# Performance work log

Measured on AMD Instinct MI355X. Metric: run time of the kernel, lower is better.

## Reference

```python
import jax, jax.numpy as jnp
import numpy as np
from jax import lax

B, S, D = 8, 1024, 128

def setup_inputs() -> dict:
    key = jax.random.key(0)
    ks = jax.random.split(key, 6)
    scale = 1.0 / np.sqrt(D)
    return {
        "x": jax.random.normal(ks[0], (B, S, D), dtype=jnp.float32),
        "Wk": jax.random.normal(ks[1], (D, D), dtype=jnp.float32) * scale,
        "Wv": jax.random.normal(ks[2], (D, D), dtype=jnp.float32) * scale,
        "Wq": jax.random.normal(ks[3], (D, D), dtype=jnp.float32) * scale,
        "Wg": jax.random.normal(ks[4], (D, 3), dtype=jnp.float32) * scale,
        "bg": jnp.zeros((3,), dtype=jnp.float32),
    }

def reference(x, Wk, Wv, Wq, Wg, bg):
    b, s, d = x.shape
    k = x @ Wk  # [b,s,d]
    v = x @ Wv
    q = x @ Wq
    gates = jax.nn.sigmoid(x @ Wg + bg)  # [b,s,3]
    alpha, eta, theta = gates[..., 0], gates[..., 1], gates[..., 2]  # [b,s]

    M0 = jnp.zeros((b, d, d), dtype=x.dtype)
    S0 = jnp.zeros((b, d, d), dtype=x.dtype)

    # time-major scan inputs
    xs = (jnp.swapaxes(k, 0, 1), jnp.swapaxes(v, 0, 1), jnp.swapaxes(q, 0, 1),
          jnp.swapaxes(alpha, 0, 1), jnp.swapaxes(eta, 0, 1), jnp.swapaxes(theta, 0, 1))

    def scan_fn(carry, inp):
        M_prev, S_prev = carry
        kt, vt, qt, at, et, tt = inp  # kt/vt/qt: [b,d]; at/et/tt: [b]
        # NOTE: original einsum 'bd,bdd->bd' takes the DIAGONAL of M (faithful)
        diagM = jnp.einsum('bdd->bd', M_prev)  # [b,d]
        yt = qt * diagM
        pred = kt * diagM
        error = pred - vt
        grad = kt[:, :, None] * error[:, None, :]  # outer product [b,d,d]
        S_new = et[:, None, None] * S_prev - tt[:, None, None] * grad
        M_new = (1.0 - at[:, None, None]) * M_prev + S_new
        return (M_new, S_new), yt

    (M_final, S_final), outputs = lax.scan(scan_fn, (M0, S0), xs)
    outputs = jnp.swapaxes(outputs, 0, 1)  # [b,s,d]
    return (outputs, (M_final, S_final))
```

## Files before the change

### kernel.cpp

```cpp
#include <hip/hip_runtime.h>
#include <math.h>

#define NB 8
#define NS 1024
#define ND 128
#define NC 64
#define NL 16

#define OFF_K  0u
#define OFF_Q  1048576u
#define OFF_V  2097152u
#define OFF_E  3145728u
#define OFF_GA 4194304u
#define OFF_GE 4202496u
#define OFF_GT 4210688u
#define OFF_W  4218880u
#define OFF_C  4227072u
#define OFF_P  4235264u

#define PL_A00 (OFF_P)
#define PL_A01 (OFF_P +  65536u)
#define PL_A10 (OFF_P + 131072u)
#define PL_A11 (OFF_P + 196608u)
#define PL_B0  (OFF_P + 262144u)
#define PL_B1  (OFF_P + 327680u)
#define PL_MST (OFF_P + 393216u)
#define PL_SST (OFF_P + 458752u)
#define PL_WCA (OFF_P + 524288u)
#define PL_WCB (OFF_P + 524800u)
#define PL_WCD (OFF_P + 525312u)
#define PL_WRQ (OFF_P + 525824u)
#define PL_WRP (OFF_P + 526336u)
#define PL_WRA (OFF_P + 526848u)
#define OFF_WT (OFF_P + 532480u)
#define WT_LO  49152u

typedef short bf16x8 __attribute__((ext_vector_type(8)));
typedef float f32x4  __attribute__((ext_vector_type(4)));

static __device__ __forceinline__ unsigned short f2bf(float f) {
    unsigned u = __builtin_bit_cast(unsigned, f);
    unsigned r = (u + 0x7FFFu + ((u >> 16) & 1u)) >> 16;
    return (unsigned short)r;
}
static __device__ __forceinline__ float bf2f(unsigned short h) {
    unsigned u = ((unsigned)h) << 16;
    return __builtin_bit_cast(float, u);
}
static __device__ __forceinline__ void split2(float a, float b,
                                              unsigned& hi, unsigned& lo) {
    unsigned short ah = f2bf(a), bh = f2bf(b);
    float ar = a - bf2f(ah), br = b - bf2f(bh);
    hi = (unsigned)ah | ((unsigned)bh << 16);
    lo = (unsigned)f2bf(ar) | ((unsigned)f2bf(br) << 16);
}

__global__ __launch_bounds__(256) void wtprep_kernel(
    const float* __restrict__ Wk, const float* __restrict__ Wv,
    const float* __restrict__ Wq, unsigned short* __restrict__ wtg)
{
    const int m    = blockIdx.x >> 4;
    const int cgrp = blockIdx.x & 15;
    const int tid  = threadIdx.x;
    const int cl   = tid >> 5;
    const int h    = tid & 31;
    const int c    = cgrp * 8 + cl;
    const float* W = (m == 0) ? Wk : (m == 1) ? Wv : Wq;

    float f[4];
#pragma unroll
    for (int i = 0; i < 4; ++i)
        f[i] = W[(h * 4 + i) * ND + c];
    uint2 hi, lo;
    split2(f[0], f[1], hi.x, lo.x);
    split2(f[2], f[3], hi.y, lo.y);
    const unsigned base = (unsigned)m * 16384u + (unsigned)c * 128u + (unsigned)h * 4u;
    *(uint2*)&wtg[base]         = hi;
    *(uint2*)&wtg[WT_LO + base] = lo;
}

__global__ __launch_bounds__(256) void proj_mfma(
    const float* __restrict__ x, const unsigned short* __restrict__ wtg,
    const float* __restrict__ Wg, const float* __restrict__ bg,
    float* __restrict__ Kb, float* __restrict__ Vb, float* __restrict__ Qb,
    float* __restrict__ ga, float* __restrict__ ge, float* __restrict__ gt)
{
    __shared__ unsigned short xs_hi[32 * 136];
    __shared__ unsigned short xs_lo[32 * 136];
    __shared__ unsigned short wt_hi[64 * 136];
    __shared__ unsigned short wt_lo[64 * 136];

    const int tid  = threadIdx.x;
    const int bid  = blockIdx.x;
    const int m    = bid >> 9;
    const int rt   = (bid >> 1) & 255;
    const int ch   = bid & 1;
    const int row0 = rt * 32;

    const float4* x4 = (const float4*)x;
#pragma unroll
    for (int l = 0; l < 4; ++l) {
        int idx = tid + l * 256;
        int r = idx >> 5, kq = idx & 31;
        float4 f = x4[(row0 + r) * 32 + kq];
        uint2 hi, lo;
        split2(f.x, f.y, hi.x, lo.x);
        split2(f.z, f.w, hi.y, lo.y);
        *(uint2*)&xs_hi[r * 136 + kq * 4] = hi;
        *(uint2*)&xs_lo[r * 136 + kq * 4] = lo;
    }
    const uint4* wh4 = (const uint4*)(wtg + m * 16384 + ch * 64 * 128);
    const uint4* wl4 = (const uint4*)(wtg + WT_LO + m * 16384 + ch * 64 * 128);
#pragma unroll
    for (int l = 0; l < 4; ++l) {
        int idx = tid + l * 256;
        int c = idx >> 4, u = idx & 15;
        *(uint4*)&wt_hi[c * 136 + u * 8] = wh4[c * 16 + u];
        *(uint4*)&wt_lo[c * 136 + u * 8] = wl4[c * 16 + u];
    }
    __syncthreads();

    const int wid  = tid >> 6;
    const int lane = tid & 63;
    const int rg   = wid >> 1;
    const int cg   = wid & 1;
    const int lrow = rg * 16 + (lane & 15);
    const int quad = lane >> 4;

    f32x4 acc[2];
    acc[0] = (f32x4){0.f, 0.f, 0.f, 0.f};
    acc[1] = (f32x4){0.f, 0.f, 0.f, 0.f};

#pragma unroll
    for (int kk = 0; kk < 4; ++kk) {
        bf16x8 ah = *(const bf16x8*)&xs_hi[lrow * 136 + kk * 32 + quad * 8];
        bf16x8 al = *(const bf16x8*)&xs_lo[lrow * 136 + kk * 32 + quad * 8];
#pragma unroll
        for (int ct = 0; ct < 2; ++ct) {
            int cl = cg * 32 + ct * 16 + (lane & 15);
            bf16x8 bh = *(const bf16x8*)&wt_hi[cl * 136 + kk * 32 + quad * 8];
            bf16x8 bl = *(const bf16x8*)&wt_lo[cl * 136 + kk * 32 + quad * 8];
            acc[ct] = __builtin_amdgcn_mfma_f32_16x16x32_bf16(ah, bh, acc[ct], 0, 0, 0);
            acc[ct] = __builtin_amdgcn_mfma_f32_16x16x32_bf16(ah, bl, acc[ct], 0, 0, 0);
            acc[ct] = __builtin_amdgcn_mfma_f32_16x16x32_bf16(al, bh, acc[ct], 0, 0, 0);
        }
    }

    float* dst = (m == 0) ? Kb : (m == 1) ? Vb : Qb;
#pragma unroll
    for (int ct = 0; ct < 2; ++ct) {
        int ocol = ch * 64 + cg * 32 + ct * 16 + (lane & 15);
#pragma unroll
        for (int r4 = 0; r4 < 4; ++r4) {
            int orow = row0 + rg * 16 + quad * 4 + r4;
            dst[orow * ND + ocol] = acc[ct][r4];
        }
    }

    if (m == 0 && ch == 0 && tid < 96) {
        int r = tid / 3, j = tid % 3;
        float z = bg[j];
        const float* xr = x + (row0 + r) * ND;
#pragma unroll 4
        for (int i = 0; i < ND; ++i)
            z = fmaf(xr[i], Wg[i * 3 + j], z);
        float gate = 1.0f / (1.0f + expf(-z));
        int row = row0 + r;
        float* gd = (j == 0) ? ga : (j == 1) ? ge : gt;
        gd[row] = gate;
    }
}

__global__ __launch_bounds__(128) void scan_phase1(
    const float* __restrict__ Kb, const float* __restrict__ Vb,
    const float* __restrict__ ga, const float* __restrict__ ge,
    const float* __restrict__ gt, float* __restrict__ ws)
{
    __shared__ float la[NL], le[NL], lt[NL];
    const int tid = threadIdx.x;
    const int b   = blockIdx.x >> 6;
    const int c   = blockIdx.x & 63;
    const int t0  = c * NL;
    const int g0  = b * NS + t0;

    if (tid < 16)       la[tid]      = ga[g0 + tid];
    else if (tid < 32)  le[tid - 16] = ge[g0 + tid - 16];
    else if (tid < 48)  lt[tid - 32] = gt[g0 + tid - 32];
    __syncthreads();

    const int d = tid;
    float A00 = 1.f, A01 = 0.f, A10 = 0.f, A11 = 1.f, B0 = 0.f, B1 = 0.f;
    int base = g0 * ND + d;
#pragma unroll
    for (int t = 0; t < NL; ++t) {
        float k = Kb[base], v = Vb[base];
        float a = la[t], e = le[t], th = lt[t];
        float tk = th * k;
        float gg = -tk * k;
        float h  = tk * v;
        float p  = (1.0f - a) + gg;
        float u0 = e * A10;
        float u1 = e * A11;
        float u2 = fmaf(e, B1, h);
        float n00 = fmaf(p, A00, u0), n10 = fmaf(gg, A00, u0);
        float n01 = fmaf(p, A01, u1), n11 = fmaf(gg, A01, u1);
        float nb0 = fmaf(p, B0, u2),  nb1 = fmaf(gg, B0, u2);
        A00 = n00; A01 = n01; A10 = n10; A11 = n11; B0 = nb0; B1 = nb1;
        base += ND;
    }
    const int pidx = (b * NC + c) * ND + d;
    ws[PL_A00 + pidx] = A00;
    ws[PL_A01 + pidx] = A01;
    ws[PL_A10 + pidx] = A10;
    ws[PL_A11 + pidx] = A11;
    ws[PL_B0  + pidx] = B0;
    ws[PL_B1  + pidx] = B1;

    if (tid == 0) {
        float al = 1.f, be = 1.f, de = 0.f;
#pragma unroll
        for (int t = NL - 1; t >= 0; --t) {
            float e1 = le[t];
            float o1 = 1.0f - la[t];
            de = fmaf(e1, de, o1 * be);
            al *= e1;
            be *= o1;
        }
        ws[PL_WCA + b * NC + c] = al;
        ws[PL_WCB + b * NC + c] = be;
        ws[PL_WCD + b * NC + c] = de;
    }
}

__global__ __launch_bounds__(64) void scan_phase2(float* __restrict__ ws)
{
    const int tid = threadIdx.x;
    if (blockIdx.x < 16) {
        const int b = blockIdx.x >> 1;
        const int d = (blockIdx.x & 1) * 64 + tid;
        float m = 0.f, s = 0.f;
        int idx = (b * NC) * ND + d;
#pragma unroll 4
        for (int c = 0; c < NC; ++c) {
            ws[PL_MST + idx] = m;
            ws[PL_SST + idx] = s;
            float A00 = ws[PL_A00 + idx], A01 = ws[PL_A01 + idx];
            float A10 = ws[PL_A10 + idx], A11 = ws[PL_A11 + idx];
            float B0  = ws[PL_B0  + idx], B1  = ws[PL_B1  + idx];
            float nm = fmaf(A00, m, fmaf(A01, s, B0));
            float ns = fmaf(A10, m, fmaf(A11, s, B1));
            m = nm; s = ns;
            idx += ND;
        }
    } else if (tid < 8) {
        const int b = tid;
        float Qp = 1.f, P = 1.f, A = 1.f;
        for (int c = NC - 1; c >= 0; --c) {
            ws[PL_WRQ + b * NC + c] = Qp;
            ws[PL_WRP + b * NC + c] = P;
            ws[PL_WRA + b * NC + c] = A;
            float al = ws[PL_WCA + b * NC + c];
            float be = ws[PL_WCB + b * NC + c];
            float de = ws[PL_WCD + b * NC + c];
            float nA = fmaf(al, A, de * P);
            Qp *= al; P *= be; A = nA;
        }
    }
}

__global__ __launch_bounds__(128) void scan_phase3(
    const float* __restrict__ Kb, const float* __restrict__ Vb,
    const float* __restrict__ Qb,
    const float* __restrict__ ga, const float* __restrict__ ge,
    const float* __restrict__ gt,
    float* __restrict__ out, float* __restrict__ errb,
    float* __restrict__ wb,  float* __restrict__ cb,
    float* __restrict__ ws)
{
    __shared__ float la[NL], le[NL], lt[NL];
    const int tid = threadIdx.x;
    const int b   = blockIdx.x >> 6;
    const int c   = blockIdx.x & 63;
    const int t0  = c * NL;
    const int g0  = b * NS + t0;

    if (tid < 16)       la[tid]      = ga[g0 + tid];
    else if (tid < 32)  le[tid - 16] = ge[g0 + tid - 16];
    else if (tid < 48)  lt[tid - 32] = gt[g0 + tid - 32];
    __syncthreads();

    const int d = tid;
    const int pidx = (b * NC + c) * ND + d;
    float m = ws[PL_MST + pidx];
    float s = ws[PL_SST + pidx];
    int base = g0 * ND + d;
#pragma unroll
    for (int t = 0; t < NL; ++t) {
        float k = Kb[base], v = Vb[base], q = Qb[base];
        float a = la[t], e = le[t], th = lt[t];
        float err = fmaf(k, m, -v);
        out[base]  = q * m;
        errb[base] = err;
        float tk = th * k;
        float u  = fmaf(-(tk * k), m, tk * v);
        s = fmaf(e, s, u);
        m = fmaf(1.0f - a, m, s);
        base += ND;
    }

    if (tid == 0) {
        float Qp = ws[PL_WRQ + b * NC + c];
        float P  = ws[PL_WRP + b * NC + c];
        float A  = ws[PL_WRA + b * NC + c];
#pragma unroll
        for (int t = NL - 1; t >= 0; --t) {
            wb[g0 + t] = -lt[t] * Qp;
            cb[g0 + t] = -lt[t] * A;
            float e1 = le[t];
            float o1 = 1.0f - la[t];
            Qp *= e1;
            P  *= o1;
            A   = fmaf(e1, A, P);
        }
    }
}

__global__ __launch_bounds__(256) void finalgemm_kernel(
    const float* __restrict__ Kb, const float* __restrict__ errb,
    const float* __restrict__ wb, const float* __restrict__ cb,
    float* __restrict__ outMS)
{
    __shared__ float ks[64 * 16];
    __shared__ float wcs[64 * 2];
    const int tid = threadIdx.x;
    const int bid = blockIdx.x;
    const int b   = bid >> 7;
    const int tc  = (bid >> 3) & 15;
    const int rg  = bid & 7;
    const int bt0 = b * NS + tc * 64;

    {
        int tl = tid >> 2, r4 = tid & 3;
        *(float4*)&ks[tl * 16 + r4 * 4] =
            *(const float4*)&Kb[(bt0 + tl) * ND + rg * 16 + r4 * 4];
    }
    if (tid < 64) {
        wcs[tid * 2]     = wb[bt0 + tid];
        wcs[tid * 2 + 1] = cb[bt0 + tid];
    }
    __syncthreads();

    const int j = tid & 127;
    const int h = tid >> 7;
    float accM[8], accS[8];
#pragma unroll
    for (int i = 0; i < 8; ++i) { accM[i] = 0.f; accS[i] = 0.f; }

    int ebase = bt0 * ND + j;
#pragma unroll 4
    for (int t = 0; t < 64; ++t) {
        float ej = errb[ebase];
        float2 wc = *(const float2*)&wcs[t * 2];
        float wej = wc.x * ej, cej = wc.y * ej;
        float4 k0 = *(const float4*)&ks[t * 16 + h * 8];
        float4 k1 = *(const float4*)&ks[t * 16 + h * 8 + 4];
        accS[0] = fmaf(k0.x, wej, accS[0]); accM[0] = fmaf(k0.x, cej, accM[0]);
        accS[1] = fmaf(k0.y, wej, accS[1]); accM[1] = fmaf(k0.y, cej, accM[1]);
        accS[2] = fmaf(k0.z, wej, accS[2]); accM[2] = fmaf(k0.z, cej, accM[2]);
        accS[3] = fmaf(k0.w, wej, accS[3]); accM[3] = fmaf(k0.w, cej, accM[3]);
        accS[4] = fmaf(k1.x, wej, accS[4]); accM[4] = fmaf(k1.x, cej, accM[4]);
        accS[5] = fmaf(k1.y, wej, accS[5]); accM[5] = fmaf(k1.y, cej, accM[5]);
        accS[6] = fmaf(k1.z, wej, accS[6]); accM[6] = fmaf(k1.z, cej, accM[6]);
        accS[7] = fmaf(k1.w, wej, accS[7]); accM[7] = fmaf(k1.w, cej, accM[7]);
        ebase += ND;
    }

    const int robase = rg * 16 + h * 8;
#pragma unroll
    for (int i = 0; i < 8; ++i) {
        int off = b * (ND * ND) + (robase + i) * ND + j;
        atomicAdd(&outMS[off], accM[i]);
        atomicAdd(&outMS[131072u + off], accS[i]);
    }
}

extern "C" void kernel_launch(void* const* d_in, const int* in_sizes, int n_in,
                              void* d_out, int out_size, void* d_ws, size_t ws_size,
                              hipStream_t stream) {
    const float* x  = (const float*)d_in[0];
    const float* Wk = (const float*)d_in[1];
    const float* Wv = (const float*)d_in[2];
    const float* Wq = (const float*)d_in[3];
    const float* Wg = (const float*)d_in[4];
    const float* bg = (const float*)d_in[5];
    float* out = (float*)d_out;
    float* ws  = (float*)d_ws;

    float* Kb  = ws + OFF_K;
    float* Qb  = ws + OFF_Q;
    float* Vb  = ws + OFF_V;
    float* Eb  = ws + OFF_E;
    float* ga  = ws + OFF_GA;
    float* ge  = ws + OFF_GE;
    float* gt  = ws + OFF_GT;
    float* wbf = ws + OFF_W;
    float* cbf = ws + OFF_C;
    unsigned short* wtg = (unsigned short*)(ws + OFF_WT);

    hipMemsetAsync(out + 1048576u, 0, 262144u * sizeof(float), stream);

    wtprep_kernel<<<48, 256, 0, stream>>>(Wk, Wv, Wq, wtg);
    proj_mfma<<<1536, 256, 0, stream>>>(x, wtg, Wg, bg,
                                        Kb, Vb, Qb, ga, ge, gt);
    scan_phase1<<<NB * NC, 128, 0, stream>>>(Kb, Vb, ga, ge, gt, ws);
    scan_phase2<<<17, 64, 0, stream>>>(ws);
    scan_phase3<<<NB * NC, 128, 0, stream>>>(Kb, Vb, Qb, ga, ge, gt,
                                             out, Eb, wbf, cbf, ws);
    finalgemm_kernel<<<1024, 256, 0, stream>>>(Kb, Eb, wbf, cbf,
                                               out + 1048576u);
}
```

Baseline: 119.0 us.

## Fuse scan phases and final GEMM into one cooperative kernel with grid syncs

Replaces the separate scan_phase1/2/3 and finalgemm launches with a single cooperative kernel of 512 blocks that uses grid.sync between phases. K/V/Q values are kept in registers from phase 1 to phase 3, and the output memset is folded into wtprep. The final reduction is retiled so each block covers 32 rows instead of 16. This removes launch overhead and repeated K/V loads, but adds grid-wide barrier costs, raises register pressure, and leaves half of each block's threads idle during the scan phases.

```diff
diff --git a/kernel.cpp b/kernel.cpp
--- a/kernel.cpp
+++ b/kernel.cpp
@@ -1,5 +1,8 @@
 #include <hip/hip_runtime.h>
+#include <hip/hip_cooperative_groups.h>
 #include <math.h>
+
+namespace cg = cooperative_groups;
 
 #define NB 8
 #define NS 1024
@@ -57,7 +60,8 @@
 
 __global__ __launch_bounds__(256) void wtprep_kernel(
     const float* __restrict__ Wk, const float* __restrict__ Wv,
-    const float* __restrict__ Wq, unsigned short* __restrict__ wtg)
+    const float* __restrict__ Wq, unsigned short* __restrict__ wtg,
+    float* __restrict__ outMS)
 {
     const int m    = blockIdx.x >> 4;
     const int cgrp = blockIdx.x & 15;
@@ -77,6 +81,14 @@
     const unsigned base = (unsigned)m * 16384u + (unsigned)c * 128u + (unsigned)h * 4u;
     *(uint2*)&wtg[base]         = hi;
     *(uint2*)&wtg[WT_LO + base] = lo;
+
+    const int gidx = blockIdx.x * 256 + tid;
+    const float4 z = {0.f, 0.f, 0.f, 0.f};
+#pragma unroll
+    for (int l = 0; l < 6; ++l) {
+        int i4 = gidx + l * 12288;
+        if (i4 < 65536) ((float4*)outMS)[i4] = z;
+    }
 }
 
 __global__ __launch_bounds__(256) void proj_mfma(
@@ -171,15 +183,25 @@
     }
 }
 
-__global__ __launch_bounds__(128) void scan_phase1(
+__global__ __launch_bounds__(256, 2) void fused_scan(
     const float* __restrict__ Kb, const float* __restrict__ Vb,
+    const float* __restrict__ Qb,
     const float* __restrict__ ga, const float* __restrict__ ge,
-    const float* __restrict__ gt, float* __restrict__ ws)
+    const float* __restrict__ gt,
+    float* __restrict__ out, float* __restrict__ errb,
+    float* __restrict__ wb,  float* __restrict__ cb,
+    float* __restrict__ ws,  float* __restrict__ outMS)
 {
     __shared__ float la[NL], le[NL], lt[NL];
+    __shared__ float ks[64 * 32];
+    __shared__ float wcs[64 * 2];
+
+    cg::grid_group grid = cg::this_grid();
+
     const int tid = threadIdx.x;
-    const int b   = blockIdx.x >> 6;
-    const int c   = blockIdx.x & 63;
+    const int bid = blockIdx.x;
+    const int b   = bid >> 6;
+    const int c   = bid & 63;
     const int t0  = c * NL;
     const int g0  = b * NS + t0;
 
@@ -188,34 +210,36 @@
     else if (tid < 48)  lt[tid - 32] = gt[g0 + tid - 32];
     __syncthreads();
 
-    const int d = tid;
-    float A00 = 1.f, A01 = 0.f, A10 = 0.f, A11 = 1.f, B0 = 0.f, B1 = 0.f;
-    int base = g0 * ND + d;
-#pragma unroll
-    for (int t = 0; t < NL; ++t) {
-        float k = Kb[base], v = Vb[base];
-        float a = la[t], e = le[t], th = lt[t];
-        float tk = th * k;
-        float gg = -tk * k;
-        float h  = tk * v;
-        float p  = (1.0f - a) + gg;
-        float u0 = e * A10;
-        float u1 = e * A11;
-        float u2 = fmaf(e, B1, h);
-        float n00 = fmaf(p, A00, u0), n10 = fmaf(gg, A00, u0);
-        float n01 = fmaf(p, A01, u1), n11 = fmaf(gg, A01, u1);
-        float nb0 = fmaf(p, B0, u2),  nb1 = fmaf(gg, B0, u2);
-        A00 = n00; A01 = n01; A10 = n10; A11 = n11; B0 = nb0; B1 = nb1;
-        base += ND;
-    }
-    const int pidx = (b * NC + c) * ND + d;
-    ws[PL_A00 + pidx] = A00;
-    ws[PL_A01 + pidx] = A01;
-    ws[PL_A10 + pidx] = A10;
-    ws[PL_A11 + pidx] = A11;
-    ws[PL_B0  + pidx] = B0;
-    ws[PL_B1  + pidx] = B1;
-
+    float k[NL], v[NL], q[NL];
+    if (tid < 128) {
+        const int d = tid;
+        float A00 = 1.f, A01 = 0.f, A10 = 0.f, A11 = 1.f, B0 = 0.f, B1 = 0.f;
+        int base = g0 * ND + d;
+#pragma unroll
+        for (int t = 0; t < NL; ++t) {
+            k[t] = Kb[base]; v[t] = Vb[base]; q[t] = Qb[base];
+            float a = la[t], e = le[t], th = lt[t];
+            float tk = th * k[t];
+            float gg = -tk * k[t];
+            float h  = tk * v[t];
+            float p  = (1.0f - a) + gg;
+            float u0 = e * A10;
+            float u1 = e * A11;
+            float u2 = fmaf(e, B1, h);
+            float n00 = fmaf(p, A00, u0), n10 = fmaf(gg, A00, u0);
+            float n01 = fmaf(p, A01, u1), n11 = fmaf(gg, A01, u1);
+            float nb0 = fmaf(p, B0, u2),  nb1 = fmaf(gg, B0, u2);
+            A00 = n00; A01 = n01; A10 = n10; A11 = n11; B0 = nb0; B1 = nb1;
+            base += ND;
+        }
+        const int pidx = (b * NC + c) * ND + d;
+        ws[PL_A00 + pidx] = A00;
+        ws[PL_A01 + pidx] = A01;
+        ws[PL_A10 + pidx] = A10;
+        ws[PL_A11 + pidx] = A11;
+        ws[PL_B0  + pidx] = B0;
+        ws[PL_B1  + pidx] = B1;
+    }
     if (tid == 0) {
         float al = 1.f, be = 1.f, de = 0.f;
 #pragma unroll
@@ -230,84 +254,64 @@
         ws[PL_WCB + b * NC + c] = be;
         ws[PL_WCD + b * NC + c] = de;
     }
-}
-
-__global__ __launch_bounds__(64) void scan_phase2(float* __restrict__ ws)
-{
-    const int tid = threadIdx.x;
-    if (blockIdx.x < 16) {
-        const int b = blockIdx.x >> 1;
-        const int d = (blockIdx.x & 1) * 64 + tid;
-        float m = 0.f, s = 0.f;
-        int idx = (b * NC) * ND + d;
+
+    grid.sync();
+
+    if (bid < 16) {
+        if (tid < 64) {
+            const int b2 = bid >> 1;
+            const int d  = (bid & 1) * 64 + tid;
+            float m = 0.f, s = 0.f;
+            int idx = (b2 * NC) * ND + d;
 #pragma unroll 4
-        for (int c = 0; c < NC; ++c) {
-            ws[PL_MST + idx] = m;
-            ws[PL_SST + idx] = s;
-            float A00 = ws[PL_A00 + idx], A01 = ws[PL_A01 + idx];
-            float A10 = ws[PL_A10 + idx], A11 = ws[PL_A11 + idx];
-            float B0  = ws[PL_B0  + idx], B1  = ws[PL_B1  + idx];
-            float nm = fmaf(A00, m, fmaf(A01, s, B0));
-            float ns = fmaf(A10, m, fmaf(A11, s, B1));
-            m = nm; s = ns;
-            idx += ND;
-        }
-    } else if (tid < 8) {
-        const int b = tid;
+            for (int cc = 0; cc < NC; ++cc) {
+                ws[PL_MST + idx] = m;
+                ws[PL_SST + idx] = s;
+                float A00 = ws[PL_A00 + idx], A01 = ws[PL_A01 + idx];
+                float A10 = ws[PL_A10 + idx], A11 = ws[PL_A11 + idx];
+                float B0  = ws[PL_B0  + idx], B1  = ws[PL_B1  + idx];
+                float nm = fmaf(A00, m, fmaf(A01, s, B0));
+                float ns = fmaf(A10, m, fmaf(A11, s, B1));
+                m = nm; s = ns;
+                idx += ND;
+            }
+        }
+    } else if (bid == 16 && tid < 8) {
+        const int b2 = tid;
         float Qp = 1.f, P = 1.f, A = 1.f;
-        for (int c = NC - 1; c >= 0; --c) {
-            ws[PL_WRQ + b * NC + c] = Qp;
-            ws[PL_WRP + b * NC + c] = P;
-            ws[PL_WRA + b * NC + c] = A;
-            float al = ws[PL_WCA + b * NC + c];
-            float be = ws[PL_WCB + b * NC + c];
-            float de = ws[PL_WCD + b * NC + c];
+        for (int cc = NC - 1; cc >= 0; --cc) {
+            ws[PL_WRQ + b2 * NC + cc] = Qp;
+            ws[PL_WRP + b2 * NC + cc] = P;
+            ws[PL_WRA + b2 * NC + cc] = A;
+            float al = ws[PL_WCA + b2 * NC + cc];
+            float be = ws[PL_WCB + b2 * NC + cc];
+            float de = ws[PL_WCD + b2 * NC + cc];
             float nA = fmaf(al, A, de * P);
             Qp *= al; P *= be; A = nA;
         }
     }
-}
-
-__global__ __launch_bounds__(128) void scan_phase3(
-    const float* __restrict__ Kb, const float* __restrict__ Vb,
-    const float* __restrict__ Qb,
-    const float* __restrict__ ga, const float* __restrict__ ge,
-    const float* __restrict__ gt,
-    float* __restrict__ out, float* __restrict__ errb,
-    float* __restrict__ wb,  float* __restrict__ cb,
-    float* __restrict__ ws)
-{
-    __shared__ float la[NL], le[NL], lt[NL];
-    const int tid = threadIdx.x;
-    const int b   = blockIdx.x >> 6;
-    const int c   = blockIdx.x & 63;
-    const int t0  = c * NL;
-    const int g0  = b * NS + t0;
-
-    if (tid < 16)       la[tid]      = ga[g0 + tid];
-    else if (tid < 32)  le[tid - 16] = ge[g0 + tid - 16];
-    else if (tid < 48)  lt[tid - 32] = gt[g0 + tid - 32];
-    __syncthreads();
-
-    const int d = tid;
-    const int pidx = (b * NC + c) * ND + d;
-    float m = ws[PL_MST + pidx];
-    float s = ws[PL_SST + pidx];
-    int base = g0 * ND + d;
-#pragma unroll
-    for (int t = 0; t < NL; ++t) {
-        float k = Kb[base], v = Vb[base], q = Qb[base];
-        float a = la[t], e = le[t], th = lt[t];
-        float err = fmaf(k, m, -v);
-        out[base]  = q * m;
-        errb[base] = err;
-        float tk = th * k;
-        float u  = fmaf(-(tk * k), m, tk * v);
-        s = fmaf(e, s, u);
-        m = fmaf(1.0f - a, m, s);
-        base += ND;
-    }
-
+
+    grid.sync();
+
+    if (tid < 128) {
+        const int d = tid;
+        const int pidx = (b * NC + c) * ND + d;
+        float m = ws[PL_MST + pidx];
+        float s = ws[PL_SST + pidx];
+        int base = g0 * ND + d;
+#pragma unroll
+        for (int t = 0; t < NL; ++t) {
+            float a = la[t], e = le[t], th = lt[t];
+            float err = fmaf(k[t], m, -v[t]);
+            out[base]  = q[t] * m;
+            errb[base] = err;
+            float tk = th * k[t];
+            float u  = fmaf(-(tk * k[t]), m, tk * v[t]);
+            s = fmaf(e, s, u);
+            m = fmaf(1.0f - a, m, s);
+            base += ND;
+        }
+    }
     if (tid == 0) {
         float Qp = ws[PL_WRQ + b * NC + c];
         float P  = ws[PL_WRP + b * NC + c];
@@ -323,26 +327,20 @@
             A   = fmaf(e1, A, P);
         }
     }
-}
-
-__global__ __launch_bounds__(256) void finalgemm_kernel(
-    const float* __restrict__ Kb, const float* __restrict__ errb,
-    const float* __restrict__ wb, const float* __restrict__ cb,
-    float* __restrict__ outMS)
-{
-    __shared__ float ks[64 * 16];
-    __shared__ float wcs[64 * 2];
-    const int tid = threadIdx.x;
-    const int bid = blockIdx.x;
-    const int b   = bid >> 7;
-    const int tc  = (bid >> 3) & 15;
-    const int rg  = bid & 7;
-    const int bt0 = b * NS + tc * 64;
-
-    {
-        int tl = tid >> 2, r4 = tid & 3;
-        *(float4*)&ks[tl * 16 + r4 * 4] =
-            *(const float4*)&Kb[(bt0 + tl) * ND + rg * 16 + r4 * 4];
+
+    grid.sync();
+
+    const int b2  = bid >> 6;
+    const int tc  = (bid >> 2) & 15;
+    const int rh  = bid & 3;
+    const int bt0 = b2 * NS + tc * 64;
+
+#pragma unroll
+    for (int l = 0; l < 2; ++l) {
+        int idx = tid + l * 256;
+        int tl = idx >> 3, r4 = idx & 7;
+        *(float4*)&ks[tl * 32 + r4 * 4] =
+            *(const float4*)&Kb[(bt0 + tl) * ND + rh * 32 + r4 * 4];
     }
     if (tid < 64) {
         wcs[tid * 2]     = wb[bt0 + tid];
@@ -352,33 +350,31 @@
 
     const int j = tid & 127;
     const int h = tid >> 7;
-    float accM[8], accS[8];
-#pragma unroll
-    for (int i = 0; i < 8; ++i) { accM[i] = 0.f; accS[i] = 0.f; }
+    float accM[16], accS[16];
+#pragma unroll
+    for (int i = 0; i < 16; ++i) { accM[i] = 0.f; accS[i] = 0.f; }
 
     int ebase = bt0 * ND + j;
-#pragma unroll 4
+#pragma unroll 2
     for (int t = 0; t < 64; ++t) {
         float ej = errb[ebase];
-        float2 wc = *(const float2*)&wcs[t * 2];
-        float wej = wc.x * ej, cej = wc.y * ej;
-        float4 k0 = *(const float4*)&ks[t * 16 + h * 8];
-        float4 k1 = *(const float4*)&ks[t * 16 + h * 8 + 4];
-        accS[0] = fmaf(k0.x, wej, accS[0]); accM[0] = fmaf(k0.x, cej, accM[0]);
-        accS[1] = fmaf(k0.y, wej, accS[1]); accM[1] = fmaf(k0.y, cej, accM[1]);
-        accS[2] = fmaf(k0.z, wej, accS[2]); accM[2] = fmaf(k0.z, cej, accM[2]);
-        accS[3] = fmaf(k0.w, wej, accS[3]); accM[3] = fmaf(k0.w, cej, accM[3]);
-        accS[4] = fmaf(k1.x, wej, accS[4]); accM[4] = fmaf(k1.x, cej, accM[4]);
-        accS[5] = fmaf(k1.y, wej, accS[5]); accM[5] = fmaf(k1.y, cej, accM[5]);
-        accS[6] = fmaf(k1.z, wej, accS[6]); accM[6] = fmaf(k1.z, cej, accM[6]);
-        accS[7] = fmaf(k1.w, wej, accS[7]); accM[7] = fmaf(k1.w, cej, accM[7]);
+        float2 wc2 = *(const float2*)&wcs[t * 2];
+        float wej = wc2.x * ej, cej = wc2.y * ej;
+#pragma unroll
+        for (int w = 0; w < 4; ++w) {
+            float4 kw = *(const float4*)&ks[t * 32 + h * 16 + w * 4];
+            accS[w*4+0] = fmaf(kw.x, wej, accS[w*4+0]); accM[w*4+0] = fmaf(kw.x, cej, accM[w*4+0]);
+            accS[w*4+1] = fmaf(kw.y, wej, accS[w*4+1]); accM[w*4+1] = fmaf(kw.y, cej, accM[w*4+1]);
+            accS[w*4+2] = fmaf(kw.z, wej, accS[w*4+2]); accM[w*4+2] = fmaf(kw.z, cej, accM[w*4+2]);
+            accS[w*4+3] = fmaf(kw.w, wej, accS[w*4+3]); accM[w*4+3] = fmaf(kw.w, cej, accM[w*4+3]);
+        }
         ebase += ND;
     }
 
-    const int robase = rg * 16 + h * 8;
-#pragma unroll
-    for (int i = 0; i < 8; ++i) {
-        int off = b * (ND * ND) + (robase + i) * ND + j;
+    const int rb = rh * 32 + h * 16;
+#pragma unroll
+    for (int i = 0; i < 16; ++i) {
+        int off = b2 * (ND * ND) + (rb + i) * ND + j;
         atomicAdd(&outMS[off], accM[i]);
         atomicAdd(&outMS[131072u + off], accS[i]);
     }
@@ -405,17 +401,17 @@
     float* gt  = ws + OFF_GT;
     float* wbf = ws + OFF_W;
     float* cbf = ws + OFF_C;
+    float* outMS = out + 1048576u;
     unsigned short* wtg = (unsigned short*)(ws + OFF_WT);
 
-    hipMemsetAsync(out + 1048576u, 0, 262144u * sizeof(float), stream);
-
-    wtprep_kernel<<<48, 256, 0, stream>>>(Wk, Wv, Wq, wtg);
+    wtprep_kernel<<<48, 256, 0, stream>>>(Wk, Wv, Wq, wtg, outMS);
     proj_mfma<<<1536, 256, 0, stream>>>(x, wtg, Wg, bg,
                                         Kb, Vb, Qb, ga, ge, gt);
-    scan_phase1<<<NB * NC, 128, 0, stream>>>(Kb, Vb, ga, ge, gt, ws);
-    scan_phase2<<<17, 64, 0, stream>>>(ws);
-    scan_phase3<<<NB * NC, 128, 0, stream>>>(Kb, Vb, Qb, ga, ge, gt,
-                                             out, Eb, wbf, cbf, ws);
-    finalgemm_kernel<<<1024, 256, 0, stream>>>(Kb, Eb, wbf, cbf,
-                                               out + 1048576u);
-}
+
+    void* args[] = { (void*)&Kb, (void*)&Vb, (void*)&Qb,
+                     (void*)&ga, (void*)&ge, (void*)&gt,
+                     (void*)&out, (void*)&Eb, (void*)&wbf, (void*)&cbf,
+                     (void*)&ws, (void*)&outMS };
+    hipLaunchCooperativeKernel((void*)fused_scan, dim3(512), dim3(256),
+                               args, 0, stream);
+}
```

Result: slower. 309.2 us (+159.9%).

## Fold weight prep, memset and chunk-prefix scan into neighbouring kernels

Applied to the files above, without the earlier changes.

Removes the separate weight-split kernel by having each projection block read and split its weight slice directly. It also replaces the memset with zeroing inside the projection kernel. The serial phase-2 chunk scan is dropped, and each phase-3 block recomputes its own prefix state by walking the previous chunk transforms. This cuts three launches and their serialization. In exchange, the weight split is redone by every block with strided loads, and later chunks now do up to 64 redundant sequential steps of global loads.

```diff
diff --git a/kernel.cpp b/kernel.cpp
--- a/kernel.cpp
+++ b/kernel.cpp
@@ -24,16 +24,9 @@
 #define PL_A11 (OFF_P + 196608u)
 #define PL_B0  (OFF_P + 262144u)
 #define PL_B1  (OFF_P + 327680u)
-#define PL_MST (OFF_P + 393216u)
-#define PL_SST (OFF_P + 458752u)
 #define PL_WCA (OFF_P + 524288u)
 #define PL_WCB (OFF_P + 524800u)
 #define PL_WCD (OFF_P + 525312u)
-#define PL_WRQ (OFF_P + 525824u)
-#define PL_WRP (OFF_P + 526336u)
-#define PL_WRA (OFF_P + 526848u)
-#define OFF_WT (OFF_P + 532480u)
-#define WT_LO  49152u
 
 typedef short bf16x8 __attribute__((ext_vector_type(8)));
 typedef float f32x4  __attribute__((ext_vector_type(4)));
@@ -55,35 +48,14 @@
     lo = (unsigned)f2bf(ar) | ((unsigned)f2bf(br) << 16);
 }
 
-__global__ __launch_bounds__(256) void wtprep_kernel(
+__global__ __launch_bounds__(256) void proj_all(
+    const float* __restrict__ x,
     const float* __restrict__ Wk, const float* __restrict__ Wv,
-    const float* __restrict__ Wq, unsigned short* __restrict__ wtg)
-{
-    const int m    = blockIdx.x >> 4;
-    const int cgrp = blockIdx.x & 15;
-    const int tid  = threadIdx.x;
-    const int cl   = tid >> 5;
-    const int h    = tid & 31;
-    const int c    = cgrp * 8 + cl;
-    const float* W = (m == 0) ? Wk : (m == 1) ? Wv : Wq;
-
-    float f[4];
-#pragma unroll
-    for (int i = 0; i < 4; ++i)
-        f[i] = W[(h * 4 + i) * ND + c];
-    uint2 hi, lo;
-    split2(f[0], f[1], hi.x, lo.x);
-    split2(f[2], f[3], hi.y, lo.y);
-    const unsigned base = (unsigned)m * 16384u + (unsigned)c * 128u + (unsigned)h * 4u;
-    *(uint2*)&wtg[base]         = hi;
-    *(uint2*)&wtg[WT_LO + base] = lo;
-}
-
-__global__ __launch_bounds__(256) void proj_mfma(
-    const float* __restrict__ x, const unsigned short* __restrict__ wtg,
+    const float* __restrict__ Wq,
     const float* __restrict__ Wg, const float* __restrict__ bg,
     float* __restrict__ Kb, float* __restrict__ Vb, float* __restrict__ Qb,
-    float* __restrict__ ga, float* __restrict__ ge, float* __restrict__ gt)
+    float* __restrict__ ga, float* __restrict__ ge, float* __restrict__ gt,
+    float* __restrict__ outMS)
 {
     __shared__ unsigned short xs_hi[32 * 136];
     __shared__ unsigned short xs_lo[32 * 136];
@@ -96,6 +68,14 @@
     const int rt   = (bid >> 1) & 255;
     const int ch   = bid & 1;
     const int row0 = rt * 32;
+
+    {
+        int g = bid * 256 + tid;
+        if (g < 65536) {
+            const float4 z = {0.f, 0.f, 0.f, 0.f};
+            ((float4*)outMS)[g] = z;
+        }
+    }
 
     const float4* x4 = (const float4*)x;
 #pragma unroll
@@ -109,14 +89,25 @@
         *(uint2*)&xs_hi[r * 136 + kq * 4] = hi;
         *(uint2*)&xs_lo[r * 136 + kq * 4] = lo;
     }
-    const uint4* wh4 = (const uint4*)(wtg + m * 16384 + ch * 64 * 128);
-    const uint4* wl4 = (const uint4*)(wtg + WT_LO + m * 16384 + ch * 64 * 128);
-#pragma unroll
-    for (int l = 0; l < 4; ++l) {
-        int idx = tid + l * 256;
-        int c = idx >> 4, u = idx & 15;
-        *(uint4*)&wt_hi[c * 136 + u * 8] = wh4[c * 16 + u];
-        *(uint4*)&wt_lo[c * 136 + u * 8] = wl4[c * 16 + u];
+
+    {
+        const float* W = (m == 0) ? Wk : (m == 1) ? Wv : Wq;
+        const int c  = tid & 63;
+        const int kg = tid >> 6;
+        const int gc = ch * 64 + c;
+#pragma unroll
+        for (int l = 0; l < 8; ++l) {
+            int k0 = (kg * 8 + l) * 4;
+            float f0 = W[(k0 + 0) * ND + gc];
+            float f1 = W[(k0 + 1) * ND + gc];
+            float f2 = W[(k0 + 2) * ND + gc];
+            float f3 = W[(k0 + 3) * ND + gc];
+            uint2 hi, lo;
+            split2(f0, f1, hi.x, lo.x);
+            split2(f2, f3, hi.y, lo.y);
+            *(uint2*)&wt_hi[c * 136 + k0] = hi;
+            *(uint2*)&wt_lo[c * 136 + k0] = lo;
+        }
     }
     __syncthreads();
 
@@ -232,18 +223,33 @@
     }
 }
 
-__global__ __launch_bounds__(64) void scan_phase2(float* __restrict__ ws)
+__global__ __launch_bounds__(128) void scan_phase3(
+    const float* __restrict__ Kb, const float* __restrict__ Vb,
+    const float* __restrict__ Qb,
+    const float* __restrict__ ga, const float* __restrict__ ge,
+    const float* __restrict__ gt,
+    float* __restrict__ out, float* __restrict__ errb,
+    float* __restrict__ wb,  float* __restrict__ cb,
+    const float* __restrict__ ws)
 {
+    __shared__ float la[NL], le[NL], lt[NL];
     const int tid = threadIdx.x;
-    if (blockIdx.x < 16) {
-        const int b = blockIdx.x >> 1;
-        const int d = (blockIdx.x & 1) * 64 + tid;
-        float m = 0.f, s = 0.f;
+    const int b   = blockIdx.x >> 6;
+    const int c   = blockIdx.x & 63;
+    const int t0  = c * NL;
+    const int g0  = b * NS + t0;
+
+    if (tid < 16)       la[tid]      = ga[g0 + tid];
+    else if (tid < 32)  le[tid - 16] = ge[g0 + tid - 16];
+    else if (tid < 48)  lt[tid - 32] = gt[g0 + tid - 32];
+    __syncthreads();
+
+    const int d = tid;
+
+    float m = 0.f, s = 0.f;
+    {
         int idx = (b * NC) * ND + d;
-#pragma unroll 4
-        for (int c = 0; c < NC; ++c) {
-            ws[PL_MST + idx] = m;
-            ws[PL_SST + idx] = s;
+        for (int cc = 0; cc < c; ++cc) {
             float A00 = ws[PL_A00 + idx], A01 = ws[PL_A01 + idx];
             float A10 = ws[PL_A10 + idx], A11 = ws[PL_A11 + idx];
             float B0  = ws[PL_B0  + idx], B1  = ws[PL_B1  + idx];
@@ -252,47 +258,8 @@
             m = nm; s = ns;
             idx += ND;
         }
-    } else if (tid < 8) {
-        const int b = tid;
-        float Qp = 1.f, P = 1.f, A = 1.f;
-        for (int c = NC - 1; c >= 0; --c) {
-            ws[PL_WRQ + b * NC + c] = Qp;
-            ws[PL_WRP + b * NC + c] = P;
-            ws[PL_WRA + b * NC + c] = A;
-            float al = ws[PL_WCA + b * NC + c];
-            float be = ws[PL_WCB + b * NC + c];
-            float de = ws[PL_WCD + b * NC + c];
-            float nA = fmaf(al, A, de * P);
-            Qp *= al; P *= be; A = nA;
-        }
-    }
-}
-
-__global__ __launch_bounds__(128) void scan_phase3(
-    const float* __restrict__ Kb, const float* __restrict__ Vb,
-    const float* __restrict__ Qb,
-    const float* __restrict__ ga, const float* __restrict__ ge,
-    const float* __restrict__ gt,
-    float* __restrict__ out, float* __restrict__ errb,
-    float* __restrict__ wb,  float* __restrict__ cb,
-    float* __restrict__ ws)
-{
-    __shared__ float la[NL], le[NL], lt[NL];
-    const int tid = threadIdx.x;
-    const int b   = blockIdx.x >> 6;
-    const int c   = blockIdx.x & 63;
-    const int t0  = c * NL;
-    const int g0  = b * NS + t0;
-
-    if (tid < 16)       la[tid]      = ga[g0 + tid];
-    else if (tid < 32)  le[tid - 16] = ge[g0 + tid - 16];
-    else if (tid < 48)  lt[tid - 32] = gt[g0 + tid - 32];
-    __syncthreads();
-
-    const int d = tid;
-    const int pidx = (b * NC + c) * ND + d;
-    float m = ws[PL_MST + pidx];
-    float s = ws[PL_SST + pidx];
+    }
+
     int base = g0 * ND + d;
 #pragma unroll
     for (int t = 0; t < NL; ++t) {
@@ -309,9 +276,14 @@
     }
 
     if (tid == 0) {
-        float Qp = ws[PL_WRQ + b * NC + c];
-        float P  = ws[PL_WRP + b * NC + c];
-        float A  = ws[PL_WRA + b * NC + c];
+        float Qp = 1.f, P = 1.f, A = 1.f;
+        for (int cc = NC - 1; cc > c; --cc) {
+            float al = ws[PL_WCA + b * NC + cc];
+            float be = ws[PL_WCB + b * NC + cc];
+            float de = ws[PL_WCD + b * NC + cc];
+            float nA = fmaf(al, A, de * P);
+            Qp *= al; P *= be; A = nA;
+        }
 #pragma unroll
         for (int t = NL - 1; t >= 0; --t) {
             wb[g0 + t] = -lt[t] * Qp;
@@ -405,17 +377,12 @@
     float* gt  = ws + OFF_GT;
     float* wbf = ws + OFF_W;
     float* cbf = ws + OFF_C;
-    unsigned short* wtg = (unsigned short*)(ws + OFF_WT);
-
-    hipMemsetAsync(out + 1048576u, 0, 262144u * sizeof(float), stream);
-
-    wtprep_kernel<<<48, 256, 0, stream>>>(Wk, Wv, Wq, wtg);
-    proj_mfma<<<1536, 256, 0, stream>>>(x, wtg, Wg, bg,
-                                        Kb, Vb, Qb, ga, ge, gt);
+    float* outMS = out + 1048576u;
+
+    proj_all<<<1536, 256, 0, stream>>>(x, Wk, Wv, Wq, Wg, bg,
+                                       Kb, Vb, Qb, ga, ge, gt, outMS);
     scan_phase1<<<NB * NC, 128, 0, stream>>>(Kb, Vb, ga, ge, gt, ws);
-    scan_phase2<<<17, 64, 0, stream>>>(ws);
     scan_phase3<<<NB * NC, 128, 0, stream>>>(Kb, Vb, Qb, ga, ge, gt,
                                              out, Eb, wbf, cbf, ws);
-    finalgemm_kernel<<<1024, 256, 0, stream>>>(Kb, Eb, wbf, cbf,
-                                               out + 1048576u);
-}
+    finalgemm_kernel<<<1024, 256, 0, stream>>>(Kb, Eb, wbf, cbf, outMS);
+}
```

New measurement: 124.6 us. +4.7%, slower.
